# Kernel optimization log

Hardware: AMD Instinct MI355X
Metric: run time of the kernel (lower is better)

The kernel has to match this reference:

```python
import jax, jax.numpy as jnp
import numpy as np

B, DIM, H, W = 1, 96, 192, 192
HEADS = 6
HD = DIM // HEADS
WIN = (8, 4)
STRIDE = (4, 2)
WH, WW = WIN
N = WH * WW
SCALE = HD ** -0.5
EPS = 1e-8

_hs = np.arange(0, H - WH + 1, STRIDE[0])
_ws = np.arange(0, W - WW + 1, STRIDE[1])
NH, NW = len(_hs), len(_ws)
HIDX = jnp.asarray(_hs[:, None] + np.arange(WH)[None, :])  # (NH, WH)
WIDX = jnp.asarray(_ws[:, None] + np.arange(WW)[None, :])  # (NW, WW)

# relative-position index table (N, N)
_co = np.stack(np.meshgrid(np.arange(WH), np.arange(WW), indexing='ij')).reshape(2, -1)
_rp = _co[:, :, None] - _co[:, None, :]
_rp[0] += WH - 1
_rp[1] += WW - 1
_rp[0] *= 2 * WW - 1
REL_IDX = jnp.asarray(_rp[0] + _rp[1])


def _clin(wr, wi, x):
    # complex 1x1 conv as channel matmul
    xr, xi = x.real, x.imag
    yr = jnp.einsum('oc,nchw->nohw', wr, xr) - jnp.einsum('oc,nchw->nohw', wi, xi)
    yi = jnp.einsum('oc,nchw->nohw', wr, xi) + jnp.einsum('oc,nchw->nohw', wi, xr)
    return jax.lax.complex(yr, yi)


def _bn(x, g, b):
    # BatchNorm2d in training mode: batch statistics, biased variance, eps=1e-5
    mu = x.mean(axis=(0, 2, 3), keepdims=True)
    var = ((x - mu) ** 2).mean(axis=(0, 2, 3), keepdims=True)
    return g[None, :, None, None] * (x - mu) * jax.lax.rsqrt(var + 1e-5) + b[None, :, None, None]


def _cbn(x, gr, br, gi, bi):
    return jax.lax.complex(_bn(x.real, gr, br), _bn(x.imag, gi, bi))


def _cgelu(x):
    mag = jnp.abs(x)
    return x * (jax.nn.gelu(mag, approximate=False) / (mag + EPS))


def _heads(t):
    # (Bn, H*D, wh, ww) -> (Bn, H, N, D)
    return t.reshape(-1, HEADS, HD, N).transpose(0, 1, 3, 2)


def reference(x_real, x_imag, qkv_wr, qkv_wi, proj_wr, proj_wi, rel,
              mlp1_wr, mlp1_wi, mlp2_wr, mlp2_wi,
              n1_gr, n1_br, n1_gi, n1_bi, n2_gr, n2_br, n2_gi, n2_bi):
    x = jax.lax.complex(x_real, x_imag)  # (B, C, H, W)

    # unfold: gather overlapping windows -> (B, C, NH, NW, WH, WW)
    xw = x[:, :, HIDX[:, None, :, None], WIDX[None, :, None, :]]
    xw = xw.transpose(0, 2, 3, 1, 4, 5).reshape(B * NH * NW, DIM, WH, WW)

    qkv = _clin(qkv_wr, qkv_wi, xw)
    q, k, v = jnp.split(qkv, 3, axis=1)
    q, k, v = _heads(q), _heads(k), _heads(v)

    attn = jnp.einsum('bhnd,bhmd->bhnm', q, jnp.conj(k)) * SCALE
    bias = rel[:, REL_IDX]  # (HEADS, N, N), real
    attn = attn + bias[None]
    mag = jnp.abs(attn)
    wsm = jax.nn.softmax(mag, axis=-1)
    attn = attn * (wsm / (mag + EPS))  # magnitude-softmax, phase preserved
    out = jnp.einsum('bhnm,bhmd->bhnd', attn, v)
    out = out.transpose(0, 1, 3, 2).reshape(-1, DIM, WH, WW)
    out = _clin(proj_wr, proj_wi, out)

    # fold: scatter-add windows back, then overlap-average
    out = out.reshape(B, NH, NW, DIM, WH, WW).transpose(0, 3, 1, 2, 4, 5)
    folded = jnp.zeros((B, DIM, H, W), jnp.complex64).at[
        :, :, HIDX[:, None, :, None], WIDX[None, :, None, :]].add(out)
    counts = jnp.zeros((H, W), jnp.float32).at[
        HIDX[:, None, :, None], WIDX[None, :, None, :]].add(1.0)
    x_ = folded / (counts + EPS)

    x = _cbn(x + x_, n1_gr, n1_br, n1_gi, n1_bi)
    m = _clin(mlp2_wr, mlp2_wi, _cgelu(_clin(mlp1_wr, mlp1_wi, x)))
    x = _cbn(x + m, n2_gr, n2_br, n2_gi, n2_bi)
    return jnp.stack([x.real, x.imag], axis=0)  # (2, B, C, H, W)


def setup_inputs() -> dict:
    key = jax.random.key(0)
    ks = jax.random.split(key, 11)
    n = lambda k, s: jax.random.normal(k, s, jnp.float32) * 0.02
    return {
        'x_real': jax.random.normal(ks[0], (B, DIM, H, W), jnp.float32),
        'x_imag': jax.random.normal(ks[1], (B, DIM, H, W), jnp.float32),
        'qkv_wr': n(ks[2], (3 * DIM, DIM)), 'qkv_wi': n(ks[3], (3 * DIM, DIM)),
        'proj_wr': n(ks[4], (DIM, DIM)), 'proj_wi': n(ks[5], (DIM, DIM)),
        'rel': n(ks[6], (HEADS, (2 * WH - 1) * (2 * WW - 1))),
        'mlp1_wr': n(ks[7], (4 * DIM, DIM)), 'mlp1_wi': n(ks[8], (4 * DIM, DIM)),
        'mlp2_wr': n(ks[9], (DIM, 4 * DIM)), 'mlp2_wi': n(ks[10], (DIM, 4 * DIM)),
        'n1_gr': jnp.ones(DIM), 'n1_br': jnp.zeros(DIM),
        'n1_gi': jnp.ones(DIM), 'n1_bi': jnp.zeros(DIM),
        'n2_gr': jnp.ones(DIM), 'n2_br': jnp.zeros(DIM),
        'n2_gi': jnp.ones(DIM), 'n2_bi': jnp.zeros(DIM),
    }
```

## Files before the change

### kernel.cpp

```cpp
#include <hip/hip_runtime.h>
#include <math.h>

#define PIX 36864
#define IMW 192
#define NWIN 4465
#define NWIN_W 95
#define NTASK (NWIN * 6)

typedef short bf16x8 __attribute__((ext_vector_type(8)));
typedef short bf16x4 __attribute__((ext_vector_type(4)));
typedef float floatx4 __attribute__((ext_vector_type(4)));

#if defined(__has_builtin)
#  if __has_builtin(__builtin_amdgcn_rcpf)
#    define RCP(x) __builtin_amdgcn_rcpf(x)
#  endif
#endif
#ifndef RCP
#  define RCP(x) (1.0f / (x))
#endif

__device__ __forceinline__ unsigned short f2bf(float f) {
    union { float f; unsigned u; } v; v.f = f;
    unsigned r = v.u + 0x7fff + ((v.u >> 16) & 1);
    return (unsigned short)(r >> 16);
}
__device__ __forceinline__ float bf2f(unsigned short b) {
    union { unsigned u; float f; } v; v.u = ((unsigned)b) << 16;
    return v.f;
}

__device__ __forceinline__ void emit3(
    const float* __restrict__ wr, const float* __restrict__ wi,
    unsigned short* __restrict__ outr, unsigned short* __restrict__ outi,
    unsigned short* __restrict__ outni, int e)
{
    outr[e] = f2bf(wr[e]);
    unsigned short b = f2bf(wi[e]);
    outi[e]  = b;
    outni[e] = b ^ 0x8000;
}

__global__ __launch_bounds__(256) void wconv_all_kernel(
    const float* __restrict__ qwr, const float* __restrict__ qwi,
    const float* __restrict__ pwr, const float* __restrict__ pwi,
    const float* __restrict__ w2r, const float* __restrict__ w2i,
    unsigned short* __restrict__ wq, unsigned short* __restrict__ wp,
    unsigned short* __restrict__ w2, float* __restrict__ ssum)
{
    int blk = blockIdx.x;
    if (blk == 288) {
        for (int j = threadIdx.x; j < 768; j += 256) ssum[j] = 0.f;
        return;
    }
    if (blk < 108)      emit3(qwr, qwi, wq, wq + 27648, wq + 55296, blk * 256 + threadIdx.x);
    else if (blk < 144) emit3(pwr, pwi, wp, wp + 9216,  wp + 18432, (blk - 108) * 256 + threadIdx.x);
    else                emit3(w2r, w2i, w2, w2 + 36864, w2 + 73728, (blk - 144) * 256 + threadIdx.x);
}

__global__ __launch_bounds__(256) void pack_kernel(
    const float* __restrict__ sr, const float* __restrict__ si,
    unsigned short* __restrict__ dr, unsigned short* __restrict__ di, int N)
{
    int n  = blockIdx.x * 256 + threadIdx.x;
    int kb = blockIdx.y;
    bf16x8 vr, vi;
#pragma unroll
    for (int j = 0; j < 8; ++j) {
        ((unsigned short*)&vr)[j] = f2bf(sr[(size_t)(kb * 8 + j) * N + n]);
        ((unsigned short*)&vi)[j] = f2bf(si[(size_t)(kb * 8 + j) * N + n]);
    }
    *(bf16x8*)&dr[((size_t)kb * N + n) * 8] = vr;
    *(bf16x8*)&di[((size_t)kb * N + n) * 8] = vi;
}

template<int K, int MT, int STORE>
__global__ __launch_bounds__(256, 2) void cgemm_mfma_kernel(
    const unsigned short* __restrict__ Wr, const unsigned short* __restrict__ Wi,
    const unsigned short* __restrict__ Wni,
    const unsigned short* __restrict__ Xr, const unsigned short* __restrict__ Xi,
    float* __restrict__ Yr, float* __restrict__ Yi,
    unsigned short* __restrict__ Pr, int N)
{
    const int lane = threadIdx.x & 63;
    const int wave = threadIdx.x >> 6;
    const int g = lane >> 4;
    const int r = lane & 15;
    const int m0 = (blockIdx.x % MT) * 32;
    const int n0 = (blockIdx.x / MT) * 256 + wave * 64;

    floatx4 accR[2][4], accI[2][4];
#pragma unroll
    for (int t = 0; t < 2; ++t)
#pragma unroll
        for (int j = 0; j < 4; ++j) {
            accR[t][j] = (floatx4){0.f, 0.f, 0.f, 0.f};
            accI[t][j] = (floatx4){0.f, 0.f, 0.f, 0.f};
        }

    for (int kc = 0; kc < K; kc += 32) {
        bf16x8 awr[2], awi[2], awni[2];
#pragma unroll
        for (int t = 0; t < 2; ++t) {
            size_t wb = (size_t)(m0 + t * 16 + r) * K + kc + g * 8;
            awr[t]  = *(const bf16x8*)&Wr[wb];
            awi[t]  = *(const bf16x8*)&Wi[wb];
            awni[t] = *(const bf16x8*)&Wni[wb];
        }
        bf16x8 bxr[4], bxi[4];
        const size_t krow = (size_t)((kc >> 3) + g);
#pragma unroll
        for (int j = 0; j < 4; ++j) {
            size_t off = (krow * N + n0 + j * 16 + r) * 8;
            bxr[j] = *(const bf16x8*)&Xr[off];
            bxi[j] = *(const bf16x8*)&Xi[off];
        }
#pragma unroll
        for (int t = 0; t < 2; ++t)
#pragma unroll
            for (int j = 0; j < 4; ++j) {
                accR[t][j] = __builtin_amdgcn_mfma_f32_16x16x32_bf16(awr[t],  bxr[j], accR[t][j], 0, 0, 0);
                accR[t][j] = __builtin_amdgcn_mfma_f32_16x16x32_bf16(awni[t], bxi[j], accR[t][j], 0, 0, 0);
                accI[t][j] = __builtin_amdgcn_mfma_f32_16x16x32_bf16(awr[t],  bxi[j], accI[t][j], 0, 0, 0);
                accI[t][j] = __builtin_amdgcn_mfma_f32_16x16x32_bf16(awi[t],  bxr[j], accI[t][j], 0, 0, 0);
            }
    }

    if (STORE == 0) {
#pragma unroll
        for (int t = 0; t < 2; ++t)
#pragma unroll
            for (int j = 0; j < 4; ++j) {
                int col = n0 + j * 16 + r;
#pragma unroll
                for (int reg = 0; reg < 4; ++reg) {
                    int row = m0 + t * 16 + g * 4 + reg;
                    Yr[(size_t)row * N + col] = accR[t][j][reg];
                    Yi[(size_t)row * N + col] = accI[t][j][reg];
                }
            }
    } else {
#pragma unroll
        for (int t = 0; t < 2; ++t) {
            int ch0 = m0 + t * 16;
            int which = ch0 / 96;
            int hh = (ch0 % 96) / 16;
#pragma unroll
            for (int j = 0; j < 4; ++j) {
                int col = n0 + j * 16 + r;
                bf16x4 pr, pi;
#pragma unroll
                for (int reg = 0; reg < 4; ++reg) {
                    ((unsigned short*)&pr)[reg] = f2bf(accR[t][j][reg]);
                    ((unsigned short*)&pi)[reg] = f2bf(accI[t][j][reg]);
                }
                size_t sb = (((size_t)col * 3 + which) * 6 + hh) * 32;
                *(bf16x4*)&Pr[sb + g * 4]      = pr;
                *(bf16x4*)&Pr[sb + 16 + g * 4] = pi;
            }
        }
    }
}

__global__ __launch_bounds__(256) void attn_mfma_kernel(
    const unsigned short* __restrict__ qkvb,
    const float* __restrict__ rel,
    unsigned short* __restrict__ wout)
{
    __shared__ unsigned aLDS[4][32 * 36];
    __shared__ unsigned vLDS[4][32 * 17];

    const int wv   = threadIdx.x >> 6;
    const int lane = threadIdx.x & 63;
    const int lr   = lane & 15;
    const int g    = lane >> 4;

    int t = blockIdx.x * 4 + wv;
    if (t >= NTASK) t = NTASK - 1;
    const int w = t / 6, h = t % 6;
    const int nh = w / NWIN_W, nw = w % NWIN_W;
    const int r0 = nh * 4, c0 = nw * 2;

    unsigned* AL = aLDS[wv];
    unsigned* VL = vLDS[wv];

    auto slot = [&](int p, int which) -> size_t {
        int gpix = (r0 + (p >> 2)) * IMW + c0 + (p & 3);
        return ((size_t)gpix * 18 + which * 6 + h) * 32;
    };

    {
        int m = lane & 31;
        int half = lane >> 5;
        size_t sv = slot(m, 2);
        const bf16x8 vr = *(const bf16x8*)&qkvb[sv + half * 8];
        const bf16x8 vi = *(const bf16x8*)&qkvb[sv + 16 + half * 8];
#pragma unroll
        for (int j = 0; j < 8; ++j) {
            unsigned pk = (unsigned)(unsigned short)vr[j] |
                          ((unsigned)(unsigned short)vi[j] << 16);
            VL[m * 17 + half * 8 + j] = pk;
        }
    }

    const int hoff = (g >> 1) * 16;
    const int loff = (g & 1) * 8;
    const unsigned sm = (g >= 2) ? 0x80008000u : 0u;
    bf16x8 Are[2], Aim[2], Bre[2], Bim[2];
#pragma unroll
    for (int tt = 0; tt < 2; ++tt) {
        size_t sq = slot(tt * 16 + lr, 0);
        size_t sk = slot(tt * 16 + lr, 1);
        Are[tt] = *(const bf16x8*)&qkvb[sq + hoff + loff];
        Aim[tt] = *(const bf16x8*)&qkvb[sq + (16 - hoff) + loff];
        Bre[tt] = *(const bf16x8*)&qkvb[sk + hoff + loff];
        bf16x8 tmp = Bre[tt];
        unsigned* u = (unsigned*)&tmp;
        u[0] ^= sm; u[1] ^= sm; u[2] ^= sm; u[3] ^= sm;
        Bim[tt] = tmp;
    }

    const floatx4 z4 = (floatx4){0.f, 0.f, 0.f, 0.f};
    floatx4 Sre[2][2], Sim[2][2];
#pragma unroll
    for (int tn = 0; tn < 2; ++tn)
#pragma unroll
        for (int tm = 0; tm < 2; ++tm) {
            Sre[tn][tm] = __builtin_amdgcn_mfma_f32_16x16x32_bf16(Are[tn], Bre[tm], z4, 0, 0, 0);
            Sim[tn][tm] = __builtin_amdgcn_mfma_f32_16x16x32_bf16(Aim[tn], Bim[tm], z4, 0, 0, 0);
        }

    const float* relh = rel + h * 105;
#pragma unroll
    for (int tn = 0; tn < 2; ++tn)
#pragma unroll
        for (int tm = 0; tm < 2; ++tm) {
            int m = tm * 16 + lr;
            int ym = m >> 2, xm = m & 3;
            int yn = tn * 4 + g;
            int bidx = (yn - ym + 7) * 7 + (3 - xm);
#pragma unroll
            for (int reg = 0; reg < 4; ++reg) {
                float re = Sre[tn][tm][reg] * 0.25f + relh[bidx + reg];
                float im = Sim[tn][tm][reg] * 0.25f;
                int n = tn * 16 + g * 4 + reg;
                AL[n * 36 + m] = (unsigned)f2bf(re) | ((unsigned)f2bf(im) << 16);
            }
        }
    __syncthreads();

    {
        const int row = lane & 31;
        const int half = lane >> 5;
        unsigned* rp = &AL[row * 36 + half * 16];
        unsigned pk[16];
        *(uint4*)&pk[0]  = *(const uint4*)&rp[0];
        *(uint4*)&pk[4]  = *(const uint4*)&rp[4];
        *(uint4*)&pk[8]  = *(const uint4*)&rp[8];
        *(uint4*)&pk[12] = *(const uint4*)&rp[12];
        float re[16], im[16], mg[16];
#pragma unroll
        for (int j = 0; j < 16; ++j) {
            union { unsigned u; float f; } a, b;
            a.u = pk[j] << 16;
            b.u = pk[j] & 0xffff0000u;
            re[j] = a.f; im[j] = b.f;
            mg[j] = sqrtf(a.f * a.f + b.f * b.f);
        }
        float mx = mg[0];
#pragma unroll
        for (int j = 1; j < 16; ++j) mx = fmaxf(mx, mg[j]);
        mx = fmaxf(mx, __shfl_xor(mx, 32, 64));
        float es[16], ss = 0.f;
#pragma unroll
        for (int j = 0; j < 16; ++j) { es[j] = __expf(mg[j] - mx); ss += es[j]; }
        ss += __shfl_xor(ss, 32, 64);
        float inv = RCP(ss);
#pragma unroll
        for (int j = 0; j < 16; ++j) {
            float f = es[j] * inv * RCP(mg[j] + 1e-8f);
            pk[j] = (unsigned)f2bf(re[j] * f) | ((unsigned)f2bf(im[j] * f) << 16);
        }
        *(uint4*)&rp[0]  = *(uint4*)&pk[0];
        *(uint4*)&rp[4]  = *(uint4*)&pk[4];
        *(uint4*)&rp[8]  = *(uint4*)&pk[8];
        *(uint4*)&rp[12] = *(uint4*)&pk[12];
    }
    __syncthreads();

    floatx4 Pre[2] = {z4, z4}, Pim[2] = {z4, z4};
#pragma unroll
    for (int kc = 0; kc < 2; ++kc) {
        bf16x8 Bpr, Bpi;
        unsigned* bpr = (unsigned*)&Bpr;
        unsigned* bpi = (unsigned*)&Bpi;
#pragma unroll
        for (int p = 0; p < 4; ++p) {
            unsigned pv = VL[(kc * 16 + g * 4 + p) * 17 + lr];
            bpr[p] = pv ^ 0x80000000u;
            bpi[p] = (pv >> 16) | (pv << 16);
        }
#pragma unroll
        for (int tn = 0; tn < 2; ++tn) {
            bf16x8 Af = *(bf16x8*)&AL[(tn * 16 + lr) * 36 + kc * 16 + g * 4];
            Pre[tn] = __builtin_amdgcn_mfma_f32_16x16x32_bf16(Af, Bpr, Pre[tn], 0, 0, 0);
            Pim[tn] = __builtin_amdgcn_mfma_f32_16x16x32_bf16(Af, Bpi, Pim[tn], 0, 0, 0);
        }
    }

#pragma unroll
    for (int tn = 0; tn < 2; ++tn)
#pragma unroll
        for (int reg = 0; reg < 4; ++reg) {
            int n = tn * 16 + g * 4 + reg;
            int ch = h * 16 + lr;
            unsigned pk = (unsigned)f2bf(Pre[tn][reg]) |
                          ((unsigned)f2bf(Pim[tn][reg]) << 16);
            *(unsigned*)&wout[(((size_t)w * 32 + n) * 96 + ch) * 2] = pk;
        }
}

__global__ __launch_bounds__(256) void fold_pack_kernel(
    const unsigned short* __restrict__ wout,
    unsigned short* __restrict__ dr, unsigned short* __restrict__ di)
{
    int e = blockIdx.x * 256 + threadIdx.x;
    int gpix = e / 12;
    int kb   = e % 12;
    int r = gpix / IMW, c = gpix % IMW;
    int nh0 = (r >= 7) ? ((r - 4) >> 2) : 0;
    int nh1 = min(46, r >> 2);
    int nw0 = (c >= 3) ? ((c - 2) >> 1) : 0;
    int nw1 = min(94, c >> 1);

    float accr[8] = {0,0,0,0,0,0,0,0}, acci[8] = {0,0,0,0,0,0,0,0};
    int cnt = 0;
    for (int nh = nh0; nh <= nh1; ++nh)
        for (int nw = nw0; nw <= nw1; ++nw) {
            int win = nh * NWIN_W + nw;
            int n = (r - nh * 4) * 4 + (c - nw * 2);
            const unsigned short* src = &wout[(((size_t)win * 32 + n) * 96 + kb * 8) * 2];
            bf16x8 a = *(const bf16x8*)&src[0];
            bf16x8 b = *(const bf16x8*)&src[8];
#pragma unroll
            for (int j = 0; j < 4; ++j) {
                accr[j]     += bf2f((unsigned short)a[j*2]);
                acci[j]     += bf2f((unsigned short)a[j*2+1]);
                accr[4 + j] += bf2f((unsigned short)b[j*2]);
                acci[4 + j] += bf2f((unsigned short)b[j*2+1]);
            }
            ++cnt;
        }
    float invc = 1.0f / ((float)cnt + 1e-8f);
    bf16x8 pr, pi;
#pragma unroll
    for (int j = 0; j < 8; ++j) {
        ((unsigned short*)&pr)[j] = f2bf(accr[j] * invc);
        ((unsigned short*)&pi)[j] = f2bf(acci[j] * invc);
    }
    *(bf16x8*)&dr[((size_t)kb * PIX + gpix) * 8] = pr;
    *(bf16x8*)&di[((size_t)kb * PIX + gpix) * 8] = pi;
}

__device__ __forceinline__ void reduce32_commit(
    float* st, int kb, float* __restrict__ ssum)
{
#pragma unroll
    for (int v = 0; v < 32; ++v)
#pragma unroll
        for (int msk = 1; msk < 64; msk <<= 1)
            st[v] += __shfl_xor(st[v], msk, 64);
    __shared__ float red[4][32];
    const int wv = threadIdx.x >> 6;
    if ((threadIdx.x & 63) == 0)
#pragma unroll
        for (int v = 0; v < 32; ++v) red[wv][v] = st[v];
    __syncthreads();
    if (threadIdx.x < 32) {
        float s = red[0][threadIdx.x] + red[1][threadIdx.x] +
                  red[2][threadIdx.x] + red[3][threadIdx.x];
        int ch = kb * 8 + (threadIdx.x >> 2);
        int stat = threadIdx.x & 3;
        int base = (stat < 2) ? ch : 96 + ch;
        atomicAdd(&ssum[base * 2 + (stat & 1)], s);
    }
}

__global__ __launch_bounds__(256) void combine_pack_kernel(
    const float* __restrict__ xr, const float* __restrict__ xi,
    const float* __restrict__ pr, const float* __restrict__ pi,
    unsigned short* __restrict__ dr, unsigned short* __restrict__ di,
    float* __restrict__ ssum)
{
    const int kb = blockIdx.x / 36;
    const int pb = blockIdx.x % 36;
    const int p0 = pb * 1024;
    float st[32];
#pragma unroll
    for (int v = 0; v < 32; ++v) st[v] = 0.f;

#pragma unroll
    for (int it = 0; it < 4; ++it) {
        int p = p0 + it * 256 + threadIdx.x;
        bf16x8 vr, vi;
#pragma unroll
        for (int ch = 0; ch < 8; ++ch) {
            int c = kb * 8 + ch;
            float a = xr[(size_t)c * PIX + p] + pr[(size_t)c * PIX + p];
            float b = xi[(size_t)c * PIX + p] + pi[(size_t)c * PIX + p];
            ((unsigned short*)&vr)[ch] = f2bf(a);
            ((unsigned short*)&vi)[ch] = f2bf(b);
            st[ch * 4 + 0] += a; st[ch * 4 + 1] += a * a;
            st[ch * 4 + 2] += b; st[ch * 4 + 3] += b * b;
        }
        *(bf16x8*)&dr[((size_t)kb * PIX + p) * 8] = vr;
        *(bf16x8*)&di[((size_t)kb * PIX + p) * 8] = vi;
    }
    reduce32_commit(st, kb, ssum);
}

__global__ __launch_bounds__(256) void scale_w_kernel(
    const float* __restrict__ w1r, const float* __restrict__ w1i,
    const float* __restrict__ gr, const float* __restrict__ br,
    const float* __restrict__ gi, const float* __restrict__ bi,
    const float* __restrict__ ssum1,
    unsigned short* __restrict__ W0, unsigned short* __restrict__ W1,
    unsigned short* __restrict__ W2, unsigned short* __restrict__ W3,
    float* __restrict__ biasR, float* __restrict__ biasI)
{
    const float invn = 1.0f / (float)PIX;
    int blk = blockIdx.x;
    if (blk < 576) {
        int e = blk * 256 + threadIdx.x;
        int mat = e / 36864;
        int idx = e % 36864;
        int k = idx % 96;
        float mr = ssum1[k * 2] * invn;
        float a_r = gr[k] * rsqrtf(ssum1[k * 2 + 1] * invn - mr * mr + 1e-5f);
        float mi = ssum1[(96 + k) * 2] * invn;
        float a_i = gi[k] * rsqrtf(ssum1[(96 + k) * 2 + 1] * invn - mi * mi + 1e-5f);
        float wr = w1r[idx], wi = w1i[idx];
        float v = (mat == 0) ? wr * a_r : (mat == 1) ? -wi * a_i
                : (mat == 2) ? wr * a_i : wi * a_r;
        unsigned short* dst = (mat == 0) ? W0 : (mat == 1) ? W1 : (mat == 2) ? W2 : W3;
        dst[idx] = f2bf(v);
    } else {
        int o = (blk - 576) * 256 + threadIdx.x;
        if (o >= 768) return;
        int isI = o >= 384;
        int oo = o % 384;
        float acc = 0.f;
        for (int k = 0; k < 96; ++k) {
            float mr = ssum1[k * 2] * invn;
            float a_r = gr[k] * rsqrtf(ssum1[k * 2 + 1] * invn - mr * mr + 1e-5f);
            float c_r = br[k] - a_r * mr;
            float mi = ssum1[(96 + k) * 2] * invn;
            float a_i = gi[k] * rsqrtf(ssum1[(96 + k) * 2 + 1] * invn - mi * mi + 1e-5f);
            float c_i = bi[k] - a_i * mi;
            float wr = w1r[oo * 96 + k], wi = w1i[oo * 96 + k];
            acc += isI ? (wr * c_i + wi * c_r) : (wr * c_r - wi * c_i);
        }
        (isI ? biasI : biasR)[oo] = acc;
    }
}

__global__ __launch_bounds__(256, 2) void mlp1bn_kernel(
    const unsigned short* __restrict__ W0, const unsigned short* __restrict__ W1,
    const unsigned short* __restrict__ W2, const unsigned short* __restrict__ W3,
    const float* __restrict__ biasR, const float* __restrict__ biasI,
    const unsigned short* __restrict__ Xr, const unsigned short* __restrict__ Xi,
    unsigned short* __restrict__ Pr, unsigned short* __restrict__ Pi, int N)
{
    const int lane = threadIdx.x & 63;
    const int wave = threadIdx.x >> 6;
    const int g = lane >> 4;
    const int r = lane & 15;
    const int m0 = (blockIdx.x % 12) * 32;
    const int n0 = (blockIdx.x / 12) * 256 + wave * 64;
    const int K = 96;

    floatx4 accR[2][4], accI[2][4];
#pragma unroll
    for (int t = 0; t < 2; ++t)
#pragma unroll
        for (int j = 0; j < 4; ++j) {
            accR[t][j] = (floatx4){0.f, 0.f, 0.f, 0.f};
            accI[t][j] = (floatx4){0.f, 0.f, 0.f, 0.f};
        }

    for (int kc = 0; kc < K; kc += 32) {
        bf16x8 a0[2], a1[2], a2[2], a3[2];
#pragma unroll
        for (int t = 0; t < 2; ++t) {
            size_t wb = (size_t)(m0 + t * 16 + r) * K + kc + g * 8;
            a0[t] = *(const bf16x8*)&W0[wb];
            a1[t] = *(const bf16x8*)&W1[wb];
            a2[t] = *(const bf16x8*)&W2[wb];
            a3[t] = *(const bf16x8*)&W3[wb];
        }
        bf16x8 bxr[4], bxi[4];
        const size_t krow = (size_t)((kc >> 3) + g);
#pragma unroll
        for (int j = 0; j < 4; ++j) {
            size_t off = (krow * N + n0 + j * 16 + r) * 8;
            bxr[j] = *(const bf16x8*)&Xr[off];
            bxi[j] = *(const bf16x8*)&Xi[off];
        }
#pragma unroll
        for (int t = 0; t < 2; ++t)
#pragma unroll
            for (int j = 0; j < 4; ++j) {
                accR[t][j] = __builtin_amdgcn_mfma_f32_16x16x32_bf16(a0[t], bxr[j], accR[t][j], 0, 0, 0);
                accR[t][j] = __builtin_amdgcn_mfma_f32_16x16x32_bf16(a1[t], bxi[j], accR[t][j], 0, 0, 0);
                accI[t][j] = __builtin_amdgcn_mfma_f32_16x16x32_bf16(a2[t], bxi[j], accI[t][j], 0, 0, 0);
                accI[t][j] = __builtin_amdgcn_mfma_f32_16x16x32_bf16(a3[t], bxr[j], accI[t][j], 0, 0, 0);
            }
    }

#pragma unroll
    for (int t = 0; t < 2; ++t) {
        float bR[4], bI[4];
#pragma unroll
        for (int reg = 0; reg < 4; ++reg) {
            int row = m0 + t * 16 + g * 4 + reg;
            bR[reg] = biasR[row];
            bI[reg] = biasI[row];
        }
#pragma unroll
        for (int j = 0; j < 4; ++j) {
            int col = n0 + j * 16 + r;
            size_t rowblk = (size_t)((m0 + t * 16 + g * 4) >> 3);
            int sub = (g & 1) * 4;
            bf16x4 pr, pi;
#pragma unroll
            for (int reg = 0; reg < 4; ++reg) {
                float a = accR[t][j][reg] + bR[reg];
                float b = accI[t][j][reg] + bI[reg];
                float mag = sqrtf(a * a + b * b);
                float f = (0.5f + 0.5f * erff(mag * 0.70710678118654752f)) * mag * RCP(mag + 1e-8f);
                ((unsigned short*)&pr)[reg] = f2bf(a * f);
                ((unsigned short*)&pi)[reg] = f2bf(b * f);
            }
            *(bf16x4*)&Pr[(rowblk * N + col) * 8 + sub] = pr;
            *(bf16x4*)&Pi[(rowblk * N + col) * 8 + sub] = pi;
        }
    }
}

__global__ __launch_bounds__(256) void addbn_kernel(
    const unsigned short* __restrict__ dr, const unsigned short* __restrict__ di,
    const float* __restrict__ ssum1,
    const float* __restrict__ gr, const float* __restrict__ br,
    const float* __restrict__ gi, const float* __restrict__ bi,
    const float* __restrict__ mr_, const float* __restrict__ mi_,
    unsigned short* __restrict__ s2r, unsigned short* __restrict__ s2i,
    float* __restrict__ ssum2)
{
    const int kb = blockIdx.x / 36;
    const int pb = blockIdx.x % 36;
    const int p0 = pb * 1024;
    const float invn = 1.0f / (float)PIX;

    float ar[8], cr[8], ai[8], ci[8];
#pragma unroll
    for (int ch = 0; ch < 8; ++ch) {
        int c = kb * 8 + ch;
        float mr = ssum1[c * 2] * invn;
        ar[ch] = gr[c] * rsqrtf(ssum1[c * 2 + 1] * invn - mr * mr + 1e-5f);
        cr[ch] = br[c] - ar[ch] * mr;
        float mi = ssum1[(96 + c) * 2] * invn;
        ai[ch] = gi[c] * rsqrtf(ssum1[(96 + c) * 2 + 1] * invn - mi * mi + 1e-5f);
        ci[ch] = bi[c] - ai[ch] * mi;
    }

    float st[32];
#pragma unroll
    for (int v = 0; v < 32; ++v) st[v] = 0.f;

#pragma unroll
    for (int it = 0; it < 4; ++it) {
        int p = p0 + it * 256 + threadIdx.x;
        bf16x8 s1r = *(const bf16x8*)&dr[((size_t)kb * PIX + p) * 8];
        bf16x8 s1i = *(const bf16x8*)&di[((size_t)kb * PIX + p) * 8];
#pragma unroll
        for (int ch = 0; ch < 8; ++ch) {
            int c = kb * 8 + ch;
            float vr = mr_[(size_t)c * PIX + p] + ar[ch] * bf2f((unsigned short)s1r[ch]) + cr[ch];
            float vi = mi_[(size_t)c * PIX + p] + ai[ch] * bf2f((unsigned short)s1i[ch]) + ci[ch];
            s2r[(size_t)c * PIX + p] = f2bf(vr);
            s2i[(size_t)c * PIX + p] = f2bf(vi);
            st[ch * 4 + 0] += vr; st[ch * 4 + 1] += vr * vr;
            st[ch * 4 + 2] += vi; st[ch * 4 + 3] += vi * vi;
        }
    }
    reduce32_commit(st, kb, ssum2);
}

__global__ __launch_bounds__(256) void bn_apply_kernel(
    const unsigned short* __restrict__ s2r, const unsigned short* __restrict__ s2i,
    const float* __restrict__ gr, const float* __restrict__ br,
    const float* __restrict__ gi, const float* __restrict__ bi,
    const float* __restrict__ ssum2,
    float* __restrict__ outr, float* __restrict__ outi)
{
    int e = blockIdx.x * 256 + threadIdx.x;
    if (e >= 96 * PIX) return;
    int ch = e / PIX;
    const float invn = 1.0f / (float)PIX;
    float mr = ssum2[ch * 2] * invn;
    float isr = rsqrtf(ssum2[ch * 2 + 1] * invn - mr * mr + 1e-5f);
    float mi = ssum2[(96 + ch) * 2] * invn;
    float isi = rsqrtf(ssum2[(96 + ch) * 2 + 1] * invn - mi * mi + 1e-5f);
    outr[e] = gr[ch] * (bf2f(s2r[e]) - mr) * isr + br[ch];
    outi[e] = gi[ch] * (bf2f(s2i[e]) - mi) * isi + bi[ch];
}

extern "C" void kernel_launch(void* const* d_in, const int* in_sizes, int n_in,
                              void* d_out, int out_size, void* d_ws, size_t ws_size,
                              hipStream_t stream)
{
    const float* x_r     = (const float*)d_in[0];
    const float* x_i     = (const float*)d_in[1];
    const float* qkv_wr  = (const float*)d_in[2];
    const float* qkv_wi  = (const float*)d_in[3];
    const float* proj_wr = (const float*)d_in[4];
    const float* proj_wi = (const float*)d_in[5];
    const float* rel     = (const float*)d_in[6];
    const float* mlp1_wr = (const float*)d_in[7];
    const float* mlp1_wi = (const float*)d_in[8];
    const float* mlp2_wr = (const float*)d_in[9];
    const float* mlp2_wi = (const float*)d_in[10];
    const float* n1_gr   = (const float*)d_in[11];
    const float* n1_br   = (const float*)d_in[12];
    const float* n1_gi   = (const float*)d_in[13];
    const float* n1_bi   = (const float*)d_in[14];
    const float* n2_gr   = (const float*)d_in[15];
    const float* n2_br   = (const float*)d_in[16];
    const float* n2_gi   = (const float*)d_in[17];
    const float* n2_bi   = (const float*)d_in[18];

    const size_t P = PIX;
    char* base = (char*)d_ws;

    unsigned short* Dr = (unsigned short*)base;
    unsigned short* Di = Dr + 96 * P;
    char* R = (char*)(Di + 96 * P);
    unsigned short* qkvb = (unsigned short*)R;
    unsigned short* wout = qkvb + 576 * P;
    float* A_r = (float*)R;
    float* A_i = A_r + 96 * P;
    unsigned short* hid_r = (unsigned short*)(A_i + 96 * P);
    unsigned short* hid_i = hid_r + 384 * P;
    unsigned short* Wb = wout + (size_t)NWIN * 32 * 96 * 2;

    unsigned short* wq = Wb;
    unsigned short* wp = Wb + 82944;
    unsigned short* w2 = Wb + 110592;
    unsigned short* W1s = Wb + 221184;
    float* biasR = (float*)(Wb + 368640);
    float* biasI = biasR + 384;
    float* ssum1 = biasI + 384;
    float* ssum2 = ssum1 + 384;
    unsigned short* s2r = (unsigned short*)(ssum2 + 384);
    unsigned short* s2i = s2r + 96 * P;

    float* out_r = (float*)d_out;
    float* out_i = out_r + 96 * P;

    dim3 blk(256);

    wconv_all_kernel<<<dim3(289), blk, 0, stream>>>(
        qkv_wr, qkv_wi, proj_wr, proj_wi, mlp2_wr, mlp2_wi, wq, wp, w2, ssum1);
    pack_kernel<<<dim3(144, 12), blk, 0, stream>>>(x_r, x_i, Dr, Di, PIX);
    cgemm_mfma_kernel<96, 9, 2><<<dim3(9 * 144), blk, 0, stream>>>(
        wq, wq + 27648, wq + 55296, Dr, Di, nullptr, nullptr, qkvb, PIX);
    attn_mfma_kernel<<<dim3((NTASK + 3) / 4), blk, 0, stream>>>(qkvb, rel, wout);
    fold_pack_kernel<<<dim3(1728), blk, 0, stream>>>(wout, Dr, Di);
    cgemm_mfma_kernel<96, 3, 0><<<dim3(3 * 144), blk, 0, stream>>>(
        wp, wp + 9216, wp + 18432, Dr, Di, A_r, A_i, nullptr, PIX);
    combine_pack_kernel<<<dim3(432), blk, 0, stream>>>(x_r, x_i, A_r, A_i, Dr, Di, ssum1);
    scale_w_kernel<<<dim3(579), blk, 0, stream>>>(
        mlp1_wr, mlp1_wi, n1_gr, n1_br, n1_gi, n1_bi, ssum1,
        W1s, W1s + 36864, W1s + 73728, W1s + 110592, biasR, biasI);
    mlp1bn_kernel<<<dim3(12 * 144), blk, 0, stream>>>(
        W1s, W1s + 36864, W1s + 73728, W1s + 110592, biasR, biasI,
        Dr, Di, hid_r, hid_i, PIX);
    cgemm_mfma_kernel<384, 3, 0><<<dim3(3 * 144), blk, 0, stream>>>(
        w2, w2 + 36864, w2 + 73728, hid_r, hid_i, A_r, A_i, nullptr, PIX);
    addbn_kernel<<<dim3(432), blk, 0, stream>>>(Dr, Di, ssum1,
        n1_gr, n1_br, n1_gi, n1_bi, A_r, A_i, s2r, s2i, ssum2);
    bn_apply_kernel<<<dim3(13824), blk, 0, stream>>>(s2r, s2i,
        n2_gr, n2_br, n2_gi, n2_bi, ssum2, out_r, out_i);
}
```

Before: 346.4 us.

## Fuse prep kernels, store GEMM outputs as bf16, re-layout attention output per pixel

Merges the weight-conversion and input-pack kernels into one launch. The proj and mlp2 GEMMs now write bf16 instead of fp32, which halves the write and re-read traffic into combine_pack and addbn. The attention output is now laid out per pixel with four parity slots instead of per window, so fold_pack reads contiguous per-pixel data. The bf16 intermediates add rounding error before the residual adds and BN statistics.

```diff
diff --git a/kernel.cpp b/kernel.cpp
--- a/kernel.cpp
+++ b/kernel.cpp
@@ -41,37 +41,31 @@
     outni[e] = b ^ 0x8000;
 }
 
-__global__ __launch_bounds__(256) void wconv_all_kernel(
+__global__ __launch_bounds__(256) void prep_kernel(
     const float* __restrict__ qwr, const float* __restrict__ qwi,
     const float* __restrict__ pwr, const float* __restrict__ pwi,
     const float* __restrict__ w2r, const float* __restrict__ w2i,
+    const float* __restrict__ xr,  const float* __restrict__ xi,
     unsigned short* __restrict__ wq, unsigned short* __restrict__ wp,
-    unsigned short* __restrict__ w2, float* __restrict__ ssum)
+    unsigned short* __restrict__ w2, float* __restrict__ ssum,
+    unsigned short* __restrict__ dr, unsigned short* __restrict__ di)
 {
     int blk = blockIdx.x;
-    if (blk == 288) {
-        for (int j = threadIdx.x; j < 768; j += 256) ssum[j] = 0.f;
-        return;
-    }
-    if (blk < 108)      emit3(qwr, qwi, wq, wq + 27648, wq + 55296, blk * 256 + threadIdx.x);
-    else if (blk < 144) emit3(pwr, pwi, wp, wp + 9216,  wp + 18432, (blk - 108) * 256 + threadIdx.x);
-    else                emit3(w2r, w2i, w2, w2 + 36864, w2 + 73728, (blk - 144) * 256 + threadIdx.x);
-}
-
-__global__ __launch_bounds__(256) void pack_kernel(
-    const float* __restrict__ sr, const float* __restrict__ si,
-    unsigned short* __restrict__ dr, unsigned short* __restrict__ di, int N)
-{
-    int n  = blockIdx.x * 256 + threadIdx.x;
-    int kb = blockIdx.y;
+    if (blk < 108)      { emit3(qwr, qwi, wq, wq + 27648, wq + 55296, blk * 256 + threadIdx.x); return; }
+    if (blk < 144)      { emit3(pwr, pwi, wp, wp + 9216,  wp + 18432, (blk - 108) * 256 + threadIdx.x); return; }
+    if (blk < 288)      { emit3(w2r, w2i, w2, w2 + 36864, w2 + 73728, (blk - 144) * 256 + threadIdx.x); return; }
+    if (blk == 288)     { for (int j = threadIdx.x; j < 768; j += 256) ssum[j] = 0.f; return; }
+    int e  = blk - 289;
+    int kb = e / 144;
+    int n  = (e % 144) * 256 + threadIdx.x;
     bf16x8 vr, vi;
 #pragma unroll
     for (int j = 0; j < 8; ++j) {
-        ((unsigned short*)&vr)[j] = f2bf(sr[(size_t)(kb * 8 + j) * N + n]);
-        ((unsigned short*)&vi)[j] = f2bf(si[(size_t)(kb * 8 + j) * N + n]);
-    }
-    *(bf16x8*)&dr[((size_t)kb * N + n) * 8] = vr;
-    *(bf16x8*)&di[((size_t)kb * N + n) * 8] = vi;
+        ((unsigned short*)&vr)[j] = f2bf(xr[(size_t)(kb * 8 + j) * PIX + n]);
+        ((unsigned short*)&vi)[j] = f2bf(xi[(size_t)(kb * 8 + j) * PIX + n]);
+    }
+    *(bf16x8*)&dr[((size_t)kb * PIX + n) * 8] = vr;
+    *(bf16x8*)&di[((size_t)kb * PIX + n) * 8] = vi;
 }
 
 template<int K, int MT, int STORE>
@@ -79,8 +73,7 @@
     const unsigned short* __restrict__ Wr, const unsigned short* __restrict__ Wi,
     const unsigned short* __restrict__ Wni,
     const unsigned short* __restrict__ Xr, const unsigned short* __restrict__ Xi,
-    float* __restrict__ Yr, float* __restrict__ Yi,
-    unsigned short* __restrict__ Pr, int N)
+    unsigned short* __restrict__ Pr, unsigned short* __restrict__ Pi, int N)
 {
     const int lane = threadIdx.x & 63;
     const int wave = threadIdx.x >> 6;
@@ -126,7 +119,7 @@
             }
     }
 
-    if (STORE == 0) {
+    if (STORE == 3) {
 #pragma unroll
         for (int t = 0; t < 2; ++t)
 #pragma unroll
@@ -135,8 +128,8 @@
 #pragma unroll
                 for (int reg = 0; reg < 4; ++reg) {
                     int row = m0 + t * 16 + g * 4 + reg;
-                    Yr[(size_t)row * N + col] = accR[t][j][reg];
-                    Yi[(size_t)row * N + col] = accI[t][j][reg];
+                    Pr[(size_t)row * N + col] = f2bf(accR[t][j][reg]);
+                    Pi[(size_t)row * N + col] = f2bf(accI[t][j][reg]);
                 }
             }
     } else {
@@ -180,11 +173,12 @@
     const int w = t / 6, h = t % 6;
     const int nh = w / NWIN_W, nw = w % NWIN_W;
     const int r0 = nh * 4, c0 = nw * 2;
+    const int slot = ((nh & 1) << 1) | (nw & 1);
 
     unsigned* AL = aLDS[wv];
     unsigned* VL = vLDS[wv];
 
-    auto slot = [&](int p, int which) -> size_t {
+    auto slotq = [&](int p, int which) -> size_t {
         int gpix = (r0 + (p >> 2)) * IMW + c0 + (p & 3);
         return ((size_t)gpix * 18 + which * 6 + h) * 32;
     };
@@ -192,7 +186,7 @@
     {
         int m = lane & 31;
         int half = lane >> 5;
-        size_t sv = slot(m, 2);
+        size_t sv = slotq(m, 2);
         const bf16x8 vr = *(const bf16x8*)&qkvb[sv + half * 8];
         const bf16x8 vi = *(const bf16x8*)&qkvb[sv + 16 + half * 8];
 #pragma unroll
@@ -209,8 +203,8 @@
     bf16x8 Are[2], Aim[2], Bre[2], Bim[2];
 #pragma unroll
     for (int tt = 0; tt < 2; ++tt) {
-        size_t sq = slot(tt * 16 + lr, 0);
-        size_t sk = slot(tt * 16 + lr, 1);
+        size_t sq = slotq(tt * 16 + lr, 0);
+        size_t sk = slotq(tt * 16 + lr, 1);
         Are[tt] = *(const bf16x8*)&qkvb[sq + hoff + loff];
         Aim[tt] = *(const bf16x8*)&qkvb[sq + (16 - hoff) + loff];
         Bre[tt] = *(const bf16x8*)&qkvb[sk + hoff + loff];
@@ -313,10 +307,11 @@
 #pragma unroll
         for (int reg = 0; reg < 4; ++reg) {
             int n = tn * 16 + g * 4 + reg;
+            int gpix = (r0 + (n >> 2)) * IMW + c0 + (n & 3);
             int ch = h * 16 + lr;
             unsigned pk = (unsigned)f2bf(Pre[tn][reg]) |
                           ((unsigned)f2bf(Pim[tn][reg]) << 16);
-            *(unsigned*)&wout[(((size_t)w * 32 + n) * 96 + ch) * 2] = pk;
+            *(unsigned*)&wout[(((size_t)gpix * 4 + slot) * 96 + ch) * 2] = pk;
         }
 }
 
@@ -337,9 +332,8 @@
     int cnt = 0;
     for (int nh = nh0; nh <= nh1; ++nh)
         for (int nw = nw0; nw <= nw1; ++nw) {
-            int win = nh * NWIN_W + nw;
-            int n = (r - nh * 4) * 4 + (c - nw * 2);
-            const unsigned short* src = &wout[(((size_t)win * 32 + n) * 96 + kb * 8) * 2];
+            int slot = ((nh & 1) << 1) | (nw & 1);
+            const unsigned short* src = &wout[(((size_t)gpix * 4 + slot) * 96 + kb * 8) * 2];
             bf16x8 a = *(const bf16x8*)&src[0];
             bf16x8 b = *(const bf16x8*)&src[8];
 #pragma unroll
@@ -388,7 +382,7 @@
 
 __global__ __launch_bounds__(256) void combine_pack_kernel(
     const float* __restrict__ xr, const float* __restrict__ xi,
-    const float* __restrict__ pr, const float* __restrict__ pi,
+    const unsigned short* __restrict__ pr, const unsigned short* __restrict__ pi,
     unsigned short* __restrict__ dr, unsigned short* __restrict__ di,
     float* __restrict__ ssum)
 {
@@ -406,8 +400,8 @@
 #pragma unroll
         for (int ch = 0; ch < 8; ++ch) {
             int c = kb * 8 + ch;
-            float a = xr[(size_t)c * PIX + p] + pr[(size_t)c * PIX + p];
-            float b = xi[(size_t)c * PIX + p] + pi[(size_t)c * PIX + p];
+            float a = xr[(size_t)c * PIX + p] + bf2f(pr[(size_t)c * PIX + p]);
+            float b = xi[(size_t)c * PIX + p] + bf2f(pi[(size_t)c * PIX + p]);
             ((unsigned short*)&vr)[ch] = f2bf(a);
             ((unsigned short*)&vi)[ch] = f2bf(b);
             st[ch * 4 + 0] += a; st[ch * 4 + 1] += a * a;
@@ -552,7 +546,7 @@
     const float* __restrict__ ssum1,
     const float* __restrict__ gr, const float* __restrict__ br,
     const float* __restrict__ gi, const float* __restrict__ bi,
-    const float* __restrict__ mr_, const float* __restrict__ mi_,
+    const unsigned short* __restrict__ mr_, const unsigned short* __restrict__ mi_,
     unsigned short* __restrict__ s2r, unsigned short* __restrict__ s2i,
     float* __restrict__ ssum2)
 {
@@ -585,8 +579,8 @@
 #pragma unroll
         for (int ch = 0; ch < 8; ++ch) {
             int c = kb * 8 + ch;
-            float vr = mr_[(size_t)c * PIX + p] + ar[ch] * bf2f((unsigned short)s1r[ch]) + cr[ch];
-            float vi = mi_[(size_t)c * PIX + p] + ai[ch] * bf2f((unsigned short)s1i[ch]) + ci[ch];
+            float vr = bf2f(mr_[(size_t)c * PIX + p]) + ar[ch] * bf2f((unsigned short)s1r[ch]) + cr[ch];
+            float vi = bf2f(mi_[(size_t)c * PIX + p]) + ai[ch] * bf2f((unsigned short)s1i[ch]) + ci[ch];
             s2r[(size_t)c * PIX + p] = f2bf(vr);
             s2i[(size_t)c * PIX + p] = f2bf(vi);
             st[ch * 4 + 0] += vr; st[ch * 4 + 1] += vr * vr;
@@ -647,11 +641,11 @@
     char* R = (char*)(Di + 96 * P);
     unsigned short* qkvb = (unsigned short*)R;
     unsigned short* wout = qkvb + 576 * P;
-    float* A_r = (float*)R;
-    float* A_i = A_r + 96 * P;
-    unsigned short* hid_r = (unsigned short*)(A_i + 96 * P);
+    unsigned short* pm_r = (unsigned short*)R;
+    unsigned short* pm_i = pm_r + 96 * P;
+    unsigned short* hid_r = pm_i + 96 * P;
     unsigned short* hid_i = hid_r + 384 * P;
-    unsigned short* Wb = wout + (size_t)NWIN * 32 * 96 * 2;
+    unsigned short* Wb = wout + (size_t)P * 4 * 96 * 2;
 
     unsigned short* wq = Wb;
     unsigned short* wp = Wb + 82944;
@@ -669,26 +663,26 @@
 
     dim3 blk(256);
 
-    wconv_all_kernel<<<dim3(289), blk, 0, stream>>>(
-        qkv_wr, qkv_wi, proj_wr, proj_wi, mlp2_wr, mlp2_wi, wq, wp, w2, ssum1);
-    pack_kernel<<<dim3(144, 12), blk, 0, stream>>>(x_r, x_i, Dr, Di, PIX);
+    prep_kernel<<<dim3(2017), blk, 0, stream>>>(
+        qkv_wr, qkv_wi, proj_wr, proj_wi, mlp2_wr, mlp2_wi, x_r, x_i,
+        wq, wp, w2, ssum1, Dr, Di);
     cgemm_mfma_kernel<96, 9, 2><<<dim3(9 * 144), blk, 0, stream>>>(
-        wq, wq + 27648, wq + 55296, Dr, Di, nullptr, nullptr, qkvb, PIX);
+        wq, wq + 27648, wq + 55296, Dr, Di, qkvb, nullptr, PIX);
     attn_mfma_kernel<<<dim3((NTASK + 3) / 4), blk, 0, stream>>>(qkvb, rel, wout);
     fold_pack_kernel<<<dim3(1728), blk, 0, stream>>>(wout, Dr, Di);
-    cgemm_mfma_kernel<96, 3, 0><<<dim3(3 * 144), blk, 0, stream>>>(
-        wp, wp + 9216, wp + 18432, Dr, Di, A_r, A_i, nullptr, PIX);
-    combine_pack_kernel<<<dim3(432), blk, 0, stream>>>(x_r, x_i, A_r, A_i, Dr, Di, ssum1);
+    cgemm_mfma_kernel<96, 3, 3><<<dim3(3 * 144), blk, 0, stream>>>(
+        wp, wp + 9216, wp + 18432, Dr, Di, pm_r, pm_i, PIX);
+    combine_pack_kernel<<<dim3(432), blk, 0, stream>>>(x_r, x_i, pm_r, pm_i, Dr, Di, ssum1);
     scale_w_kernel<<<dim3(579), blk, 0, stream>>>(
         mlp1_wr, mlp1_wi, n1_gr, n1_br, n1_gi, n1_bi, ssum1,
         W1s, W1s + 36864, W1s + 73728, W1s + 110592, biasR, biasI);
     mlp1bn_kernel<<<dim3(12 * 144), blk, 0, stream>>>(
         W1s, W1s + 36864, W1s + 73728, W1s + 110592, biasR, biasI,
         Dr, Di, hid_r, hid_i, PIX);
-    cgemm_mfma_kernel<384, 3, 0><<<dim3(3 * 144), blk, 0, stream>>>(
-        w2, w2 + 36864, w2 + 73728, hid_r, hid_i, A_r, A_i, nullptr, PIX);
+    cgemm_mfma_kernel<384, 3, 3><<<dim3(3 * 144), blk, 0, stream>>>(
+        w2, w2 + 36864, w2 + 73728, hid_r, hid_i, pm_r, pm_i, PIX);
     addbn_kernel<<<dim3(432), blk, 0, stream>>>(Dr, Di, ssum1,
-        n1_gr, n1_br, n1_gi, n1_bi, A_r, A_i, s2r, s2i, ssum2);
+        n1_gr, n1_br, n1_gi, n1_bi, pm_r, pm_i, s2r, s2i, ssum2);
     bn_apply_kernel<<<dim3(13824), blk, 0, stream>>>(s2r, s2i,
         n2_gr, n2_br, n2_gi, n2_bi, ssum2, out_r, out_i);
 }
```

Measured after the change: 344.0 us. No clear change (-0.7%).
